# Kernel tuning notes

Hardware: AMD Instinct MI355X
Metric: run time of the kernel (lower is better)

Reference implementation:

```python
import jax, jax.numpy as jnp
import numpy as np

BN_EPS = 1e-5


def _bn_train(x, gamma, beta):
    # BatchNorm1d over channel dim (axis=1) of [B, C, L], training-mode batch stats
    m = jnp.mean(x, axis=(0, 2), keepdims=True)
    v = jnp.var(x, axis=(0, 2), keepdims=True)  # biased, matches torch normalization
    xn = (x - m) * jax.lax.rsqrt(v + BN_EPS)
    return xn * gamma[None, :, None] + beta[None, :, None]


def setup_inputs() -> dict:
    key = jax.random.key(0)
    ks = jax.random.split(key, 9)
    B, d1, d2, dout, p1, p2 = 16, 64, 64, 64, 256, 256
    ini1 = np.sqrt(3.0 / dout / d1)
    ini2 = np.sqrt(3.0 / dout / d2)
    u = lambda k, s, ini: jax.random.uniform(k, s, jnp.float32, -ini, ini)
    return {
        "A_AP": jax.random.normal(ks[0], (B, d1, p1), jnp.float32),
        "A_UE": jax.random.normal(ks[1], (B, d1, p2), jnp.float32),
        "H": jax.random.normal(ks[2], (B, d2, p1, p2), jnp.float32),
        "Q1_AP": u(ks[3], (dout, d1), ini1),
        "Q2_AP": u(ks[4], (dout, d1), ini1),
        "Q1_UE": u(ks[5], (dout, d1), ini1),
        "Q2_UE": u(ks[6], (dout, d1), ini1),
        "P1_AP": u(ks[7], (dout, d2), ini2),
        "P1_UE": u(ks[8], (dout, d2), ini2),
        "gamma": jnp.ones((dout,), jnp.float32),
        "beta": jnp.zeros((dout,), jnp.float32),
        "permutation_size1": p1,
        "permutation_size2": p2,
        "BATCH_SIZE": B,
    }


def reference(A_AP, A_UE, H, Q1_AP, Q2_AP, Q1_UE, Q2_UE, P1_AP, P1_UE,
              gamma, beta, permutation_size1, permutation_size2, BATCH_SIZE):
    # mean-aggregations
    ue_mean = jnp.mean(A_UE, axis=-1)          # [B, d1]
    ap_mean = jnp.mean(A_AP, axis=-1)          # [B, d1]
    h_mean_ue = jnp.mean(H, axis=-1)           # [B, d2, p1]
    h_mean_ap = jnp.mean(H, axis=-2)           # [B, d2, p2]

    ap1 = jnp.einsum('od,bdp->bop', Q1_AP, A_AP)                # [B, out, p1]
    ap2 = jnp.einsum('od,bd->bo', Q2_AP, ue_mean)[:, :, None]   # [B, out, 1]
    ap3 = jnp.einsum('od,bdp->bop', P1_AP, h_mean_ue)           # [B, out, p1]
    ue1 = jnp.einsum('od,bdp->bop', Q1_UE, A_UE)                # [B, out, p2]
    ue2 = jnp.einsum('od,bd->bo', Q2_UE, ap_mean)[:, :, None]   # [B, out, 1]
    ue3 = jnp.einsum('od,bdp->bop', P1_UE, h_mean_ap)           # [B, out, p2]

    out_ap = 2.0 * ap1 + 2.0 * ap2 + 0.1 * ap3
    out_ue = 2.0 * ue1 + 2.0 * ue2 + 0.1 * ue3
    out_ap = jax.nn.relu(out_ap)
    out_ue = jax.nn.relu(out_ue)
    out_ap = _bn_train(out_ap, gamma, beta)
    out_ue = _bn_train(out_ue, gamma, beta)
    return out_ap, out_ue
```

## Files before the change

kernel.cpp:

```cpp
#include <hip/hip_runtime.h>
#include <stdint.h>

#define WS_HMUE 0
#define WS_HMAP 262144
#define WS_APM  524288
#define WS_UEM  525312
#define WS_Z    526336

__global__ __launch_bounds__(256) void k_reduce(
    const float* __restrict__ H,
    const float* __restrict__ A_AP, const float* __restrict__ A_UE,
    float* __restrict__ ws)
{
    const int bid = blockIdx.x;
    const int tid = threadIdx.x;
    const int w = tid >> 6;
    const int lane = tid & 63;

    __shared__ float lds_row[256];
    __shared__ float lds_col[1024];

    if (bid < 1024) {
        const float4* Hs = (const float4*)(H + (size_t)bid * 65536);
        float c0 = 0.f, c1 = 0.f, c2 = 0.f, c3 = 0.f;

        #pragma unroll 8
        for (int it = 0; it < 64; ++it) {
            const int row = it * 4 + w;
            float4 v = Hs[row * 64 + lane];
            c0 += v.x; c1 += v.y; c2 += v.z; c3 += v.w;
            float rs = (v.x + v.y) + (v.z + v.w);
            rs += __shfl_xor(rs, 1);
            rs += __shfl_xor(rs, 2);
            rs += __shfl_xor(rs, 4);
            rs += __shfl_xor(rs, 8);
            rs += __shfl_xor(rs, 16);
            rs += __shfl_xor(rs, 32);
            if (lane == 0) lds_row[row] = rs;
        }
        ((float4*)lds_col)[w * 64 + lane] = make_float4(c0, c1, c2, c3);
        __syncthreads();
        const float cs = lds_col[tid] + lds_col[256 + tid]
                       + lds_col[512 + tid] + lds_col[768 + tid];
        const int oidx = bid * 256 + tid;
        ws[WS_HMAP + oidx] = cs * (1.f / 256.f);
        ws[WS_HMUE + oidx] = lds_row[tid] * (1.f / 256.f);
    } else {
        const int m = bid - 1024;
        const int r = m * 4 + w;
        const bool is_ap = (r < 1024);
        const float4* src = is_ap ? (const float4*)(A_AP + r * 256)
                                  : (const float4*)(A_UE + (r - 1024) * 256);
        float4 v = src[lane];
        float s = (v.x + v.y) + (v.z + v.w);
        s += __shfl_xor(s, 1);
        s += __shfl_xor(s, 2);
        s += __shfl_xor(s, 4);
        s += __shfl_xor(s, 8);
        s += __shfl_xor(s, 16);
        s += __shfl_xor(s, 32);
        if (lane == 0) {
            if (is_ap) ws[WS_APM + r] = s * (1.f / 256.f);
            else       ws[WS_UEM + (r - 1024)] = s * (1.f / 256.f);
        }
    }
}

__global__ __launch_bounds__(256) void k_z(
    const float* __restrict__ A_AP, const float* __restrict__ A_UE,
    const float* __restrict__ Q1_AP, const float* __restrict__ Q2_AP,
    const float* __restrict__ Q1_UE, const float* __restrict__ Q2_UE,
    const float* __restrict__ P1_AP, const float* __restrict__ P1_UE,
    const float* __restrict__ hmue, const float* __restrict__ hmap,
    const float* __restrict__ apm,  const float* __restrict__ uem,
    float* __restrict__ z)
{
    const int bid = blockIdx.x;
    const int g = bid >> 8;
    const int rem = bid & 255;
    const int b = rem >> 4;
    const int o0 = (rem & 15) * 4;
    const int p = threadIdx.x;

    const float* A  = g ? A_UE : A_AP;
    const float* hm = g ? hmap : hmue;
    const float* am = g ? apm  : uem;
    const float* Q1 = g ? Q1_UE : Q1_AP;
    const float* Q2 = g ? Q2_UE : Q2_AP;
    const float* P1 = g ? P1_UE : P1_AP;

    __shared__ float s2[4];
    if (threadIdx.x < 4) {
        const float* qr = Q2 + (o0 + threadIdx.x) * 64;
        const float* ar = am + b * 64;
        float s = 0.f;
        #pragma unroll
        for (int d = 0; d < 64; ++d) s += qr[d] * ar[d];
        s2[threadIdx.x] = s;
    }
    __syncthreads();

    float accQ[4] = {0.f, 0.f, 0.f, 0.f};
    float accP[4] = {0.f, 0.f, 0.f, 0.f};
    const float* Ab = A  + (b << 14) + p;
    const float* hb = hm + (b << 14) + p;

    #pragma unroll 4
    for (int dd = 0; dd < 16; ++dd) {
        const int d0 = dd * 4;
        float a0 = Ab[(d0 + 0) * 256];
        float a1 = Ab[(d0 + 1) * 256];
        float a2 = Ab[(d0 + 2) * 256];
        float a3 = Ab[(d0 + 3) * 256];
        float h0 = hb[(d0 + 0) * 256];
        float h1 = hb[(d0 + 1) * 256];
        float h2 = hb[(d0 + 2) * 256];
        float h3 = hb[(d0 + 3) * 256];
        #pragma unroll
        for (int j = 0; j < 4; ++j) {
            const float4 q  = *(const float4*)(Q1 + (o0 + j) * 64 + d0);
            const float4 pc = *(const float4*)(P1 + (o0 + j) * 64 + d0);
            accQ[j] += q.x * a0 + q.y * a1 + q.z * a2 + q.w * a3;
            accP[j] += pc.x * h0 + pc.y * h1 + pc.z * h2 + pc.w * h3;
        }
    }

    #pragma unroll
    for (int j = 0; j < 4; ++j) {
        float zv = 2.f * (accQ[j] + s2[j]) + 0.1f * accP[j];
        zv = fmaxf(zv, 0.f);
        z[((size_t)(g * 16 + b) * 64 + (o0 + j)) * 256 + p] = zv;
    }
}

__global__ __launch_bounds__(256) void k_bn(
    const float* __restrict__ z,
    const float* __restrict__ gamma, const float* __restrict__ beta,
    float* __restrict__ out)
{
    const int g = blockIdx.x >> 6;
    const int o = blockIdx.x & 63;
    const int t = threadIdx.x;
    const int w = t >> 6;
    const int lane = t & 63;

    const float* zp = z + (size_t)g * 262144 + o * 256 + t;
    float v[16];
    float s = 0.f, q = 0.f;
    #pragma unroll
    for (int b = 0; b < 16; ++b) {
        float x = zp[b * 16384];
        v[b] = x;
        s += x;
        q += x * x;
    }
    #pragma unroll
    for (int m = 1; m <= 32; m <<= 1) {
        s += __shfl_xor(s, m);
        q += __shfl_xor(q, m);
    }
    __shared__ float ls[4], lq[4];
    if (lane == 0) { ls[w] = s; lq[w] = q; }
    __syncthreads();
    s = ls[0] + ls[1] + ls[2] + ls[3];
    q = lq[0] + lq[1] + lq[2] + lq[3];

    const float mean = s * (1.f / 4096.f);
    const float var  = q * (1.f / 4096.f) - mean * mean;
    const float rstd = rsqrtf(var + 1e-5f);
    const float scale = rstd * gamma[o];
    const float shift = beta[o] - mean * scale;

    float* op = out + (size_t)g * 262144 + o * 256 + t;
    #pragma unroll
    for (int b = 0; b < 16; ++b)
        op[b * 16384] = v[b] * scale + shift;
}

extern "C" void kernel_launch(void* const* d_in, const int* in_sizes, int n_in,
                              void* d_out, int out_size, void* d_ws, size_t ws_size,
                              hipStream_t stream)
{
    const float* A_AP  = (const float*)d_in[0];
    const float* A_UE  = (const float*)d_in[1];
    const float* H     = (const float*)d_in[2];
    const float* Q1_AP = (const float*)d_in[3];
    const float* Q2_AP = (const float*)d_in[4];
    const float* Q1_UE = (const float*)d_in[5];
    const float* Q2_UE = (const float*)d_in[6];
    const float* P1_AP = (const float*)d_in[7];
    const float* P1_UE = (const float*)d_in[8];
    const float* gamma = (const float*)d_in[9];
    const float* beta  = (const float*)d_in[10];

    float* ws = (float*)d_ws;
    float* out = (float*)d_out;

    hipLaunchKernelGGL(k_reduce, dim3(1536), dim3(256), 0, stream,
                       H, A_AP, A_UE, ws);

    hipLaunchKernelGGL(k_z, dim3(512), dim3(256), 0, stream,
                       A_AP, A_UE, Q1_AP, Q2_AP, Q1_UE, Q2_UE, P1_AP, P1_UE,
                       ws + WS_HMUE, ws + WS_HMAP, ws + WS_APM, ws + WS_UEM,
                       ws + WS_Z);

    hipLaunchKernelGGL(k_bn, dim3(128), dim3(256), 0, stream,
                       ws + WS_Z, gamma, beta, out);
}
```

Measured before the change: 397.4 us.

## Fuse BN statistics into z kernel via atomics and vectorize BN apply

The per-channel sum and sum-of-squares are now computed in the z kernel with wave shuffles and accumulated through global atomicAdd into a stats buffer, which an extra block in the reduce kernel zeroes. The BN kernel becomes a flat float4 elementwise pass over 512 blocks instead of 128 blocks that each did their own strided reduction. This removes the serialized stats reduction in the low-parallelism BN kernel, at the cost of atomic contention and float nondeterminism. The dominant cost is still the H reduction, so the overall effect is likely small.

Measured after the change: 398.9 us. No clear change (+0.4%).

```diff
diff --git a/kernel.cpp b/kernel.cpp
--- a/kernel.cpp
+++ b/kernel.cpp
@@ -5,7 +5,8 @@
 #define WS_HMAP 262144
 #define WS_APM  524288
 #define WS_UEM  525312
-#define WS_Z    526336
+#define WS_STAT 526336
+#define WS_Z    526592
 
 __global__ __launch_bounds__(256) void k_reduce(
     const float* __restrict__ H,
@@ -45,7 +46,7 @@
         const int oidx = bid * 256 + tid;
         ws[WS_HMAP + oidx] = cs * (1.f / 256.f);
         ws[WS_HMUE + oidx] = lds_row[tid] * (1.f / 256.f);
-    } else {
+    } else if (bid < 1536) {
         const int m = bid - 1024;
         const int r = m * 4 + w;
         const bool is_ap = (r < 1024);
@@ -63,6 +64,8 @@
             if (is_ap) ws[WS_APM + r] = s * (1.f / 256.f);
             else       ws[WS_UEM + (r - 1024)] = s * (1.f / 256.f);
         }
+    } else {
+        ws[WS_STAT + tid] = 0.f;
     }
 }
 
@@ -71,9 +74,7 @@
     const float* __restrict__ Q1_AP, const float* __restrict__ Q2_AP,
     const float* __restrict__ Q1_UE, const float* __restrict__ Q2_UE,
     const float* __restrict__ P1_AP, const float* __restrict__ P1_UE,
-    const float* __restrict__ hmue, const float* __restrict__ hmap,
-    const float* __restrict__ apm,  const float* __restrict__ uem,
-    float* __restrict__ z)
+    float* __restrict__ ws)
 {
     const int bid = blockIdx.x;
     const int g = bid >> 8;
@@ -81,15 +82,20 @@
     const int b = rem >> 4;
     const int o0 = (rem & 15) * 4;
     const int p = threadIdx.x;
+    const int w = p >> 6;
+    const int lane = p & 63;
 
     const float* A  = g ? A_UE : A_AP;
-    const float* hm = g ? hmap : hmue;
-    const float* am = g ? apm  : uem;
+    const float* hm = ws + (g ? WS_HMAP : WS_HMUE);
+    const float* am = ws + (g ? WS_APM  : WS_UEM);
     const float* Q1 = g ? Q1_UE : Q1_AP;
     const float* Q2 = g ? Q2_UE : Q2_AP;
     const float* P1 = g ? P1_UE : P1_AP;
+    float* z = ws + WS_Z;
+    float* stat = ws + WS_STAT;
 
     __shared__ float s2[4];
+    __shared__ float lds_s[4][4], lds_q[4][4];
     if (threadIdx.x < 4) {
         const float* qr = Q2 + (o0 + threadIdx.x) * 64;
         const float* ar = am + b * 64;
@@ -125,56 +131,65 @@
         }
     }
 
+    float zv[4];
     #pragma unroll
     for (int j = 0; j < 4; ++j) {
-        float zv = 2.f * (accQ[j] + s2[j]) + 0.1f * accP[j];
-        zv = fmaxf(zv, 0.f);
-        z[((size_t)(g * 16 + b) * 64 + (o0 + j)) * 256 + p] = zv;
+        float v = 2.f * (accQ[j] + s2[j]) + 0.1f * accP[j];
+        v = fmaxf(v, 0.f);
+        zv[j] = v;
+        z[((size_t)(g * 16 + b) * 64 + (o0 + j)) * 256 + p] = v;
+    }
+
+    #pragma unroll
+    for (int j = 0; j < 4; ++j) {
+        float s = zv[j];
+        float q = zv[j] * zv[j];
+        #pragma unroll
+        for (int m = 1; m <= 32; m <<= 1) {
+            s += __shfl_xor(s, m);
+            q += __shfl_xor(q, m);
+        }
+        if (lane == 0) { lds_s[w][j] = s; lds_q[w][j] = q; }
+    }
+    __syncthreads();
+    if (threadIdx.x < 4) {
+        const int j = threadIdx.x;
+        float s = lds_s[0][j] + lds_s[1][j] + lds_s[2][j] + lds_s[3][j];
+        float q = lds_q[0][j] + lds_q[1][j] + lds_q[2][j] + lds_q[3][j];
+        const int go = g * 64 + (o0 + j);
+        atomicAdd(&stat[go * 2 + 0], s);
+        atomicAdd(&stat[go * 2 + 1], q);
     }
 }
 
 __global__ __launch_bounds__(256) void k_bn(
-    const float* __restrict__ z,
+    const float* __restrict__ ws,
     const float* __restrict__ gamma, const float* __restrict__ beta,
     float* __restrict__ out)
 {
-    const int g = blockIdx.x >> 6;
-    const int o = blockIdx.x & 63;
-    const int t = threadIdx.x;
-    const int w = t >> 6;
-    const int lane = t & 63;
-
-    const float* zp = z + (size_t)g * 262144 + o * 256 + t;
-    float v[16];
-    float s = 0.f, q = 0.f;
-    #pragma unroll
-    for (int b = 0; b < 16; ++b) {
-        float x = zp[b * 16384];
-        v[b] = x;
-        s += x;
-        q += x * x;
-    }
-    #pragma unroll
-    for (int m = 1; m <= 32; m <<= 1) {
-        s += __shfl_xor(s, m);
-        q += __shfl_xor(q, m);
-    }
-    __shared__ float ls[4], lq[4];
-    if (lane == 0) { ls[w] = s; lq[w] = q; }
-    __syncthreads();
-    s = ls[0] + ls[1] + ls[2] + ls[3];
-    q = lq[0] + lq[1] + lq[2] + lq[3];
-
+    const int tid = threadIdx.x;
+    const size_t flatw = (size_t)blockIdx.x * 1024 + (tid >> 6) * 256;
+    const int g = (int)(flatw >> 18);
+    const int o = (int)((flatw >> 8) & 63);
+
+    const float* stat = ws + WS_STAT;
+    const float s = stat[(g * 64 + o) * 2 + 0];
+    const float q = stat[(g * 64 + o) * 2 + 1];
     const float mean = s * (1.f / 4096.f);
     const float var  = q * (1.f / 4096.f) - mean * mean;
     const float rstd = rsqrtf(var + 1e-5f);
     const float scale = rstd * gamma[o];
     const float shift = beta[o] - mean * scale;
 
-    float* op = out + (size_t)g * 262144 + o * 256 + t;
-    #pragma unroll
-    for (int b = 0; b < 16; ++b)
-        op[b * 16384] = v[b] * scale + shift;
+    const float4* zp = (const float4*)(ws + WS_Z);
+    const size_t i4 = (size_t)blockIdx.x * 256 + tid;
+    float4 v = zp[i4];
+    float4 r;
+    r.x = v.x * scale + shift;
+    r.y = v.y * scale + shift;
+    r.z = v.z * scale + shift;
+    r.w = v.w * scale + shift;
+    ((float4*)out)[i4] = r;
 }
 
 extern "C" void kernel_launch(void* const* d_in, const int* in_sizes, int n_in,
@@ -196,14 +211,12 @@
     float* ws = (float*)d_ws;
     float* out = (float*)d_out;
 
-    hipLaunchKernelGGL(k_reduce, dim3(1536), dim3(256), 0, stream,
+    hipLaunchKernelGGL(k_reduce, dim3(1537), dim3(256), 0, stream,
                        H, A_AP, A_UE, ws);
 
     hipLaunchKernelGGL(k_z, dim3(512), dim3(256), 0, stream,
-                       A_AP, A_UE, Q1_AP, Q2_AP, Q1_UE, Q2_UE, P1_AP, P1_UE,
-                       ws + WS_HMUE, ws + WS_HMAP, ws + WS_APM, ws + WS_UEM,
-                       ws + WS_Z);
-
-    hipLaunchKernelGGL(k_bn, dim3(128), dim3(256), 0, stream,
-                       ws + WS_Z, gamma, beta, out);
-}
+                       A_AP, A_UE, Q1_AP, Q2_AP, Q1_UE, Q2_UE, P1_AP, P1_UE, ws);
+
+    hipLaunchKernelGGL(k_bn, dim3(512), dim3(256), 0, stream,
+                       ws, gamma, beta, out);
+}
```
